# Optimization experiments

Measured on AMD Instinct MI355X. Metric: run time of the kernel, lower is better.

The kernel has to match this reference:

```python
import jax, jax.numpy as jnp
import numpy as np

# (left, right, top, bottom) zero-pad offsets for the 8 neighbors (matches nn.ZeroPad2d order in source)
PADS = [(0, 2, 0, 2), (1, 1, 0, 2), (2, 0, 0, 2), (0, 2, 1, 1),
        (2, 0, 1, 1), (0, 2, 2, 0), (1, 1, 2, 0), (2, 0, 2, 0)]
CROP_H = [96, 128, 160, 192]
CROP_W = [192, 256, 320, 384]
PROP_TIME = 3


def _shift_pad8(x):
    # x: [B,1,h,w] -> [B,8,h+2,w+2], each channel a differently shifted zero-padded copy
    xs = [jnp.pad(x[:, 0], ((0, 0), (t, b), (l, r))) for (l, r, t, b) in PADS]
    return jnp.stack(xs, axis=1)


def _cspn(guidance, blur_depth, sparse_depth):
    # guidance: [B,8,h,w]; blur_depth/sparse_depth: [B,1,h,w]. norm_type='8sum'.
    gates = [jnp.pad(guidance[:, k], ((0, 0), (t, b), (l, r)))
             for k, (l, r, t, b) in enumerate(PADS)]
    gate_wb = jnp.stack(gates, axis=1)                              # [B,8,h+2,w+2]
    abs_weight = jnp.sum(jnp.abs(gate_wb), axis=1, keepdims=True)   # [B,1,h+2,w+2]
    gate_wb = gate_wb / abs_weight
    gate_sum = jnp.sum(gate_wb, axis=1, keepdims=True)[:, :, 1:-1, 1:-1]  # [B,1,h,w]

    sparse_mask = jnp.sign(sparse_depth)
    raw = blur_depth
    result = blur_depth
    for i in range(PROP_TIME):
        if i == 0:
            result = (1.0 - sparse_mask) * result + sparse_mask * sparse_depth
        neigh = jnp.sum(gate_wb * _shift_pad8(result), axis=1, keepdims=True)
        result = (1.0 - gate_sum) * raw + neigh[:, :, 1:-1, 1:-1]
    return result


def _conv_block(x, w, b):
    # ConvBlock (monodepth2 style): reflection pad 1 + 3x3 conv + ELU
    xp = jnp.pad(x, ((0, 0), (0, 0), (1, 1), (1, 1)), mode='reflect')
    y = jax.lax.conv_general_dilated(xp, w, (1, 1), 'VALID',
                                     dimension_numbers=('NCHW', 'OIHW', 'NCHW'))
    return jax.nn.elu(y + b[None, :, None, None])


def _center_crop(x, h, w):
    oh, ow = x.shape[2], x.shape[3]
    hs = max(int(round((oh - h) / 2)), 0)
    ws = max(int(round((ow - w) / 2)), 0)
    return x[:, :, hs:min(hs + h, oh), ws:min(ws + w, ow)]


def _stage_pad(depth, h, w):
    hs, ws = depth.shape[2], depth.shape[3]
    ph, pw = (h - hs) // 2, (w - ws) // 2
    return jnp.pad(depth, ((0, 0), (0, 0), (ph, ph), (pw, pw)))


def _masked_median(x, mask):
    # torch.median semantics: lower median of the masked elements
    s = jnp.sort(jnp.where(mask, x, jnp.inf).ravel())
    n = jnp.sum(mask)
    return jnp.take(s, (n - 1) // 2)


def _stage_forward(features, rgbd, dep_last, w, b, h, wd):
    rgbd_c = _center_crop(rgbd, h, wd)
    feat_c = _center_crop(features, h, wd)
    dep = rgbd_c[:, 0:1]                       # channel 0, as in source
    mask = jnp.sign(dep_last)
    dep_fusion = dep_last * mask + dep * (1.0 - mask)
    guided_map = _conv_block(feat_c, w, b)     # [B,8,h,wd]
    x = _cspn(guided_map, dep_fusion, dep_last)
    return jnp.clip(x, 0.0, 1.0)


def setup_inputs() -> dict:
    key = jax.random.key(0)
    ks = jax.random.split(key, 12)
    B, H, W = 16, 256, 512
    inp = {
        'features': jax.random.normal(ks[0], (B, 16, H, W), jnp.float32),
        'blur_depth': jax.random.uniform(ks[1], (B, 1, H, W), jnp.float32),
        'gt': jax.random.uniform(ks[2], (B, 1, H, W), jnp.float32),
        'rgb': jax.random.uniform(ks[3], (B, 3, H, W), jnp.float32),
        'stage': jnp.arange(4, dtype=jnp.int64 if jax.config.jax_enable_x64 else jnp.int32),
    }
    scale = 1.0 / np.sqrt(16 * 9)
    for i in range(4):
        inp[f'w{i}'] = jax.random.normal(ks[4 + i], (8, 16, 3, 3), jnp.float32) * scale
        inp[f'b{i}'] = jax.random.normal(ks[8 + i], (8,), jnp.float32) * 0.01
    return inp


def reference(features, blur_depth, gt, rgb, w0, b0, w1, b1, w2, b2, w3, b3, stage):
    stage_list = [int(s) for s in np.asarray(stage)]
    gt_pos = gt > 0
    scale = _masked_median(gt, gt_pos) / _masked_median(blur_depth, gt_pos)
    all_scale = gt / blur_depth
    blur_depth_o = blur_depth * scale
    gt = jnp.where((all_scale > 1.2) | (all_scale < 0.8), 0.0, gt)
    rgbd = jnp.concatenate([rgb, blur_depth_o], axis=1)
    dep_last = _center_crop(gt, 96, 192)

    params = [(w0, b0), (w1, b1), (w2, b2), (w3, b3)]
    out = None
    for index, i in enumerate(stage_list):
        w, b = params[i]
        if index == len(stage_list) - 1:
            out = _stage_forward(features, rgbd, dep_last, w, b, CROP_H[i], CROP_W[i])
        else:
            ref_last = jax.lax.stop_gradient(
                _stage_forward(features, rgbd, dep_last, w, b, CROP_H[i], CROP_W[i]))
            dep_last = _stage_pad(ref_last, CROP_H[i + 1], CROP_W[i + 1])
    return out
```

## Files before the change

kernel.cpp:

```cpp
#include <hip/hip_runtime.h>
#include <math.h>


#define B 16
#define FH 256
#define FW 512
#define TH 32
#define TW 32
#define HALO 3
#define LD 38
#define GD 36
#define MAXC 6

typedef __attribute__((ext_vector_type(8))) short short8;
typedef __attribute__((ext_vector_type(4))) float f32x4;

__device__ __forceinline__ int swzslot(int cc, int h) {
  return (((cc << 1) | h) ^ (cc & 1) ^ ((cc >> 1) & 2));
}

__global__ __launch_bounds__(256) void prep_all_kernel(
    const float* __restrict__ gt, const float* __restrict__ blur,
    const float* __restrict__ rgb, const float* __restrict__ w0c,
    const float* __restrict__ w1c, const float* __restrict__ w2c,
    const float* __restrict__ w3c, short8* __restrict__ wf,
    float* __restrict__ r0, float* __restrict__ r1, float* __restrict__ r2,
    float* __restrict__ r3) {
  if (blockIdx.x == 0 && threadIdx.x < 64) {
    int lane = threadIdx.x;
    int px = lane & 15, g = lane >> 4;
    const float* Ws[4] = {w0c, w1c, w2c, w3c};
    for (int st = 0; st < 4; ++st) {
      const float* wgt = Ws[st];
      for (int t = 0; t < 5; ++t) {
        short8 wh, wl;
        for (int j = 0; j < 8; ++j) {
          int k = 32 * t + 8 * g + j;
          int s = k >> 4, ci = k & 15;
          float wv = 0.0f;
          if (px < 8 && s < 9) wv = wgt[(px * 16 + ci) * 9 + s];
          uint uw = __float_as_uint(wv);
          uint hw_ = (uw + 0x8000u) & 0xFFFF0000u;
          float wlo = wv - __uint_as_float(hw_);
          wh[j] = (short)(hw_ >> 16);
          wl[j] = (short)((__float_as_uint(wlo) + 0x8000u) >> 16);
        }
        wf[((st * 5 + t) * 2 + 0) * 64 + lane] = wh;
        wf[((st * 5 + t) * 2 + 1) * 64 + lane] = wl;
      }
    }
  }

  int idx = blockIdx.x * blockDim.x + threadIdx.x;
  const int n0 = B * 96 * 192, n1 = B * 128 * 256, n2 = B * 160 * 320,
            n3 = B * 192 * 384;
  float* dst;
  int h, w, hs, ws;
  if (idx < n0) {
    dst = r0; h = 96; w = 192; hs = 80; ws = 160;
  } else if (idx < n0 + n1) {
    idx -= n0; dst = r1; h = 128; w = 256; hs = 64; ws = 128;
  } else if (idx < n0 + n1 + n2) {
    idx -= n0 + n1; dst = r2; h = 160; w = 320; hs = 48; ws = 96;
  } else if (idx < n0 + n1 + n2 + n3) {
    idx -= n0 + n1 + n2; dst = r3; h = 192; w = 384; hs = 32; ws = 64;
  } else {
    return;
  }
  int x = idx % w;
  int t = idx / w;
  int y = t % h;
  int b = t / h;
  size_t g = (size_t)b * FH * FW + (size_t)(hs + y) * FW + (ws + x);
  float dep = rgb[((size_t)b * 3) * FH * FW + (size_t)(hs + y) * FW + (ws + x)];
  if (dst == r0) {
    float gv = gt[g];
    float s = gv / blur[g];
    float dl = (s > 1.2f || s < 0.8f) ? 0.0f : gv;
    dst[idx] = (dl > 0.0f) ? dl : dep;
  } else {
    dst[idx] = dep;
  }
}

__global__ __launch_bounds__(256) void conv_mfma_kernel(
    const float* __restrict__ feat, const short8* __restrict__ wf,
    const float* __restrict__ b0c, float* __restrict__ g0,
    const float* __restrict__ b1c, float* __restrict__ g1,
    const float* __restrict__ b2c, float* __restrict__ g2,
    const float* __restrict__ b3c, float* __restrict__ g3) {
  __shared__ uint4 sH[18 * 72];
  __shared__ uint4 sL[18 * 72];

  int bid = blockIdx.x;
  int h, w, base, st;
  const float* bias;
  float* guid;
  if (bid < 576)       { h = 96;  w = 192; bias = b0c; guid = g0; base = 0;    st = 0; }
  else if (bid < 1600) { h = 128; w = 256; bias = b1c; guid = g1; base = 576;  st = 1; }
  else if (bid < 3200) { h = 160; w = 320; bias = b2c; guid = g2; base = 1600; st = 2; }
  else                 { h = 192; w = 384; bias = b3c; guid = g3; base = 3200; st = 3; }
  int hs = (FH - h) >> 1, wss = (FW - w) >> 1;

  int lb = bid - base;
  int nbx = w >> 5;
  int bx = lb % nbx;
  int rem = lb / nbx;
  int nby = h >> 4;
  int by = rem % nby;
  int b = rem / nby;
  int tx0 = bx << 5, ty0 = by << 4;

  int tid = threadIdx.x;
  int lane = tid & 63, wv = tid >> 6;
  int px = lane & 15, g = lane >> 4;
  int h_ = g & 1, gb = g >> 1;

  const short8* wfs = wf + st * 640;
  short8 WH[5], WL[5];
#pragma unroll
  for (int t = 0; t < 5; ++t) {
    WH[t] = wfs[(t * 2 + 0) * 64 + lane];
    WL[t] = wfs[(t * 2 + 1) * 64 + lane];
  }
  float bias4[4];
  {
    const float* bp = bias + ((g & 1) << 2);
#pragma unroll
    for (int r = 0; r < 4; ++r) bias4[r] = bp[r];
  }

  const size_t FHW = (size_t)FH * FW;
  const float* fb = feat + (size_t)b * 16 * FHW;
  for (int u = tid; u < 612; u += 256) {
    int rr = u / 34, cc = u % 34;
    int yy = ty0 + rr - 1;
    yy = (yy < 0) ? 1 : ((yy >= h) ? h - 2 : yy);
    int xx = tx0 + cc - 1;
    xx = (xx < 0) ? 1 : ((xx >= w) ? w - 2 : xx);
    const float* fp = fb + (size_t)(hs + yy) * FW + (wss + xx);
    uint hiD[8], loD[8];
#pragma unroll
    for (int i = 0; i < 8; ++i) {
      float a0 = fp[(size_t)(2 * i) * FHW];
      float a1 = fp[(size_t)(2 * i + 1) * FHW];
      uint u0 = __float_as_uint(a0), u1 = __float_as_uint(a1);
      uint h0 = (u0 + 0x8000u) & 0xFFFF0000u;
      uint h1 = (u1 + 0x8000u) & 0xFFFF0000u;
      float l0 = a0 - __uint_as_float(h0);
      float l1 = a1 - __uint_as_float(h1);
      hiD[i] = (h0 >> 16) | h1;
      loD[i] = ((__float_as_uint(l0) + 0x8000u) >> 16) |
               (((__float_as_uint(l1) + 0x8000u) >> 16) << 16);
    }
    int r72 = rr * 72;
    sH[r72 + swzslot(cc, 0)] = make_uint4(hiD[0], hiD[1], hiD[2], hiD[3]);
    sH[r72 + swzslot(cc, 1)] = make_uint4(hiD[4], hiD[5], hiD[6], hiD[7]);
    sL[r72 + swzslot(cc, 0)] = make_uint4(loD[0], loD[1], loD[2], loD[3]);
    sL[r72 + swzslot(cc, 1)] = make_uint4(loD[4], loD[5], loD[6], loD[7]);
  }
  __syncthreads();

  size_t hw = (size_t)h * w;
  const short8* pH = (const short8*)sH;
  const short8* pL = (const short8*)sL;

  const int dyE_[5] = {-1, -1, 0, 1, 1};
  const int dxE_[5] = {-1, 1, 0, -1, 1};
  const int dyO_[5] = {-1, 0, 0, 1, 0};
  const int dxO_[5] = {0, -1, 1, 0, 0};

  for (int i = 0; i < 8; ++i) {
    int tau = wv * 8 + i;
    int row = tau >> 1, xt = tau & 1;
    int rr0 = row + 1;
    int cc0 = (xt << 4) + px + 1;
    f32x4 acc = {bias4[0], bias4[1], bias4[2], bias4[3]};
#pragma unroll
    for (int t = 0; t < 5; ++t) {
      int dy = gb ? dyO_[t] : dyE_[t];
      int dx = gb ? dxO_[t] : dxE_[t];
      int idx = (rr0 + dy) * 72 + swzslot(cc0 + dx, h_);
      short8 fh = pH[idx];
      short8 fl = pL[idx];
      acc = __builtin_amdgcn_mfma_f32_16x16x32_bf16(WH[t], fh, acc, 0, 0, 0);
      acc = __builtin_amdgcn_mfma_f32_16x16x32_bf16(WH[t], fl, acc, 0, 0, 0);
      acc = __builtin_amdgcn_mfma_f32_16x16x32_bf16(WL[t], fh, acc, 0, 0, 0);
    }
    if (g < 2) {
      int y = ty0 + row, x = tx0 + (xt << 4) + px;
      float* gp = guid + (size_t)b * 8 * hw + (size_t)y * w + x;
#pragma unroll
      for (int r = 0; r < 4; ++r) {
        int oo = g * 4 + r;
        float v = acc[r];
        v = (v > 0.0f) ? v : (__expf(v) - 1.0f);
        gp[(size_t)oo * hw] = v;
      }
    }
  }
}

__global__ __launch_bounds__(256) void cspn3_kernel(
    const float* __restrict__ guid, const float* __restrict__ raw,
    const float* __restrict__ rgb, float* __restrict__ dst, int h, int w,
    int hs, int wss, int h2, int w2, int ph, int pw, int last) {
  __shared__ float sraw[LD * LD];
  __shared__ float s0[LD * LD];
  __shared__ float s1[LD * LD];

  int tpw = w / TW, tph = h / TH;
  int tile = blockIdx.x;
  int tx = tile % tpw;
  int t2 = tile / tpw;
  int ty = t2 % tph;
  int b = t2 / tph;
  int oy = ty * TH - HALO, ox = tx * TW - HALO;
  int tid = threadIdx.x;

  const float* rb = raw + (size_t)b * h * w;

  for (int e = tid; e < LD * LD; e += 256) {
    int r = e / LD, c = e % LD;
    int gy = oy + r, gx = ox + c;
    bool in = (gy >= 0 && gy < h && gx >= 0 && gx < w);
    sraw[e] = in ? rb[(size_t)gy * w + gx] : 0.0f;
  }
  __syncthreads();

  const int dy8[8] = {1, 1, 1, 0, 0, -1, -1, -1};
  const int dx8[8] = {1, 0, -1, 1, -1, 1, 0, -1};
  const int off8[8] = {LD + 1, LD, LD - 1, 1, -1, -LD + 1, -LD, -LD - 1};

  const float* gb = guid + (size_t)b * 8 * h * w;
  float cg[MAXC][8];
  float r0[MAXC];
  int adr[MAXC];
#pragma unroll
  for (int ch = 0; ch < MAXC; ++ch) {
    int p = tid + ch * 256;
    bool ok = p < GD * GD;
    int pp = ok ? p : 0;
    int py = pp / GD + 1, px = pp % GD + 1;
    adr[ch] = py * LD + px;
    int gy = oy + py, gx = ox + px;
    bool in = ok && gy >= 0 && gy < h && gx >= 0 && gx < w;
    float wsum = 0.0f, asum = 0.0f;
    float g[8];
#pragma unroll
    for (int k = 0; k < 8; ++k) {
      int ny = gy + dy8[k], nx = gx + dx8[k];
      bool nin = ok && ny >= 0 && ny < h && nx >= 0 && nx < w;
      float gk = nin ? gb[(size_t)k * h * w + (size_t)ny * w + nx] : 0.0f;
      g[k] = gk;
      wsum += gk;
      asum += fabsf(gk);
    }
    float inv = in ? (1.0f / asum) : 0.0f;
#pragma unroll
    for (int k = 0; k < 8; ++k) cg[ch][k] = g[k] * inv;
    r0[ch] = in ? (1.0f - wsum * inv) * sraw[adr[ch]] : 0.0f;
  }

#pragma unroll
  for (int ch = 0; ch < MAXC; ++ch) {
    int p = tid + ch * 256;
    if (p < GD * GD) {
      float v = r0[ch];
#pragma unroll
      for (int k = 0; k < 8; ++k) v += cg[ch][k] * sraw[adr[ch] + off8[k]];
      s0[adr[ch]] = v;
    }
  }
  __syncthreads();

#pragma unroll
  for (int ch = 0; ch < MAXC; ++ch) {
    int p = tid + ch * 256;
    if (p < GD * GD) {
      int py = p / GD + 1, px = p % GD + 1;
      if (py >= 2 && py <= 35 && px >= 2 && px <= 35) {
        float v = r0[ch];
#pragma unroll
        for (int k = 0; k < 8; ++k) v += cg[ch][k] * s0[adr[ch] + off8[k]];
        s1[adr[ch]] = v;
      }
    }
  }
  __syncthreads();

#pragma unroll
  for (int ch = 0; ch < MAXC; ++ch) {
    int p = tid + ch * 256;
    if (p < GD * GD) {
      int py = p / GD + 1, px = p % GD + 1;
      if (py >= 3 && py <= 34 && px >= 3 && px <= 34) {
        float v = r0[ch];
#pragma unroll
        for (int k = 0; k < 8; ++k) v += cg[ch][k] * s1[adr[ch] + off8[k]];
        float dl = fminf(fmaxf(v, 0.0f), 1.0f);
        int gy = oy + py, gx = ox + px;
        if (last) {
          dst[((size_t)b * h + gy) * w + gx] = dl;
        } else {
          float dep = rgb[((size_t)b * 3) * FH * FW + (size_t)(hs + gy) * FW +
                          (wss + gx)];
          dst[((size_t)b * h2 + (gy + ph)) * w2 + (gx + pw)] =
              (dl > 0.0f) ? dl : dep;
        }
      }
    }
  }
}

extern "C" void kernel_launch(void* const* d_in, const int* in_sizes, int n_in,
                              void* d_out, int out_size, void* d_ws,
                              size_t ws_size, hipStream_t stream) {
  (void)in_sizes; (void)n_in; (void)out_size; (void)ws_size;
  const float* feat = (const float*)d_in[0];
  const float* blur = (const float*)d_in[1];
  const float* gt = (const float*)d_in[2];
  const float* rgb = (const float*)d_in[3];
  const float* W[4] = {(const float*)d_in[5], (const float*)d_in[7],
                       (const float*)d_in[9], (const float*)d_in[11]};
  const float* Bs[4] = {(const float*)d_in[6], (const float*)d_in[8],
                        (const float*)d_in[10], (const float*)d_in[12]};
  float* out = (float*)d_out;

  float* G0 = (float*)d_ws;
  float* G1 = G0 + (size_t)B * 8 * 96 * 192;
  float* G2 = G1 + (size_t)B * 8 * 128 * 256;
  float* G3 = G2 + (size_t)B * 8 * 160 * 320;
  float* RAW[4];
  RAW[0] = G3 + (size_t)B * 8 * 192 * 384;
  RAW[1] = RAW[0] + (size_t)B * 96 * 192;
  RAW[2] = RAW[1] + (size_t)B * 128 * 256;
  RAW[3] = RAW[2] + (size_t)B * 160 * 320;
  short8* WF = (short8*)(RAW[3] + (size_t)B * 192 * 384);
  float* G[4] = {G0, G1, G2, G3};

  const int CH[4] = {96, 128, 160, 192};
  const int CW[4] = {192, 256, 320, 384};

  {
    int n = B * (96 * 192 + 128 * 256 + 160 * 320 + 192 * 384);
    prep_all_kernel<<<(n + 255) / 256, 256, 0, stream>>>(
        gt, blur, rgb, W[0], W[1], W[2], W[3], WF, RAW[0], RAW[1], RAW[2],
        RAW[3]);
  }

  conv_mfma_kernel<<<5504, 256, 0, stream>>>(feat, WF, Bs[0], G0, Bs[1], G1,
                                             Bs[2], G2, Bs[3], G3);

  for (int i = 0; i < 4; ++i) {
    int h = CH[i], w = CW[i];
    int hs = (FH - h) / 2, wss = (FW - w) / 2;
    int ntiles = B * (h / TH) * (w / TW);
    if (i < 3) {
      int h2 = CH[i + 1], w2 = CW[i + 1];
      int ph = (h2 - h) / 2, pw = (w2 - w) / 2;
      cspn3_kernel<<<ntiles, 256, 0, stream>>>(G[i], RAW[i], rgb, RAW[i + 1],
                                               h, w, hs, wss, h2, w2, ph, pw,
                                               0);
    } else {
      cspn3_kernel<<<ntiles, 256, 0, stream>>>(G[i], RAW[i], rgb, out, h, w,
                                               hs, wss, h, w, 0, 0, 1);
    }
  }
}
```

Before: 183.9 us.

## Share feature tile loads across all four stage convolutions

The conv kernel now launches one block per tile of the largest 192x384 crop instead of separate blocks per stage. Each block loads and splits the feature halo into shared memory once, then runs the convolution for every stage whose crop fully contains the tile. Reflection padding at each stage's borders is handled by remapping neighbour indices inside the stencil. This removes redundant global feature reads across the nested crops, but central blocks now do up to four convolutions each, so work per block becomes uneven.

Result: faster. 173.2 us (-5.8%).

```diff
diff --git a/kernel.cpp b/kernel.cpp
--- a/kernel.cpp
+++ b/kernel.cpp
@@ -93,52 +93,26 @@
   __shared__ uint4 sL[18 * 72];
 
   int bid = blockIdx.x;
-  int h, w, base, st;
-  const float* bias;
-  float* guid;
-  if (bid < 576)       { h = 96;  w = 192; bias = b0c; guid = g0; base = 0;    st = 0; }
-  else if (bid < 1600) { h = 128; w = 256; bias = b1c; guid = g1; base = 576;  st = 1; }
-  else if (bid < 3200) { h = 160; w = 320; bias = b2c; guid = g2; base = 1600; st = 2; }
-  else                 { h = 192; w = 384; bias = b3c; guid = g3; base = 3200; st = 3; }
-  int hs = (FH - h) >> 1, wss = (FW - w) >> 1;
-
-  int lb = bid - base;
-  int nbx = w >> 5;
-  int bx = lb % nbx;
-  int rem = lb / nbx;
-  int nby = h >> 4;
-  int by = rem % nby;
-  int b = rem / nby;
-  int tx0 = bx << 5, ty0 = by << 4;
+  int bx = bid % 12;
+  int t0 = bid / 12;
+  int by = t0 % 12;
+  int b = t0 / 12;
+  int ty0 = by << 4, tx0 = bx << 5;
 
   int tid = threadIdx.x;
   int lane = tid & 63, wv = tid >> 6;
   int px = lane & 15, g = lane >> 4;
   int h_ = g & 1, gb = g >> 1;
-
-  const short8* wfs = wf + st * 640;
-  short8 WH[5], WL[5];
-#pragma unroll
-  for (int t = 0; t < 5; ++t) {
-    WH[t] = wfs[(t * 2 + 0) * 64 + lane];
-    WL[t] = wfs[(t * 2 + 1) * 64 + lane];
-  }
-  float bias4[4];
-  {
-    const float* bp = bias + ((g & 1) << 2);
-#pragma unroll
-    for (int r = 0; r < 4; ++r) bias4[r] = bp[r];
-  }
 
   const size_t FHW = (size_t)FH * FW;
   const float* fb = feat + (size_t)b * 16 * FHW;
   for (int u = tid; u < 612; u += 256) {
     int rr = u / 34, cc = u % 34;
     int yy = ty0 + rr - 1;
-    yy = (yy < 0) ? 1 : ((yy >= h) ? h - 2 : yy);
+    yy = (yy < 0) ? 0 : ((yy > 191) ? 191 : yy);
     int xx = tx0 + cc - 1;
-    xx = (xx < 0) ? 1 : ((xx >= w) ? w - 2 : xx);
-    const float* fp = fb + (size_t)(hs + yy) * FW + (wss + xx);
+    xx = (xx < 0) ? 0 : ((xx > 383) ? 383 : xx);
+    const float* fp = fb + (size_t)(32 + yy) * FW + (64 + xx);
     uint hiD[8], loD[8];
 #pragma unroll
     for (int i = 0; i < 8; ++i) {
@@ -161,41 +135,78 @@
   }
   __syncthreads();
 
-  size_t hw = (size_t)h * w;
   const short8* pH = (const short8*)sH;
   const short8* pL = (const short8*)sL;
-
   const int dyE_[5] = {-1, -1, 0, 1, 1};
   const int dxE_[5] = {-1, 1, 0, -1, 1};
   const int dyO_[5] = {-1, 0, 0, 1, 0};
   const int dxO_[5] = {0, -1, 1, 0, 0};
 
-  for (int i = 0; i < 8; ++i) {
-    int tau = wv * 8 + i;
-    int row = tau >> 1, xt = tau & 1;
-    int rr0 = row + 1;
-    int cc0 = (xt << 4) + px + 1;
-    f32x4 acc = {bias4[0], bias4[1], bias4[2], bias4[3]};
+  const int SH[4] = {96, 128, 160, 192};
+  const int SW[4] = {192, 256, 320, 384};
+  const int OY[4] = {48, 32, 16, 0};
+  const int OX[4] = {96, 64, 32, 0};
+  const float* BIAS[4] = {b0c, b1c, b2c, b3c};
+  float* GD_[4] = {g0, g1, g2, g3};
+
+#pragma unroll
+  for (int st = 0; st < 4; ++st) {
+    int sh = SH[st], sw = SW[st], oy = OY[st], ox = OX[st];
+    bool inR = (ty0 >= oy) && (ty0 + 16 <= oy + sh) && (tx0 >= ox) &&
+               (tx0 + 32 <= ox + sw);
+    if (!inR) continue;
+    bool topE = (ty0 == oy), botE = (ty0 + 16 == oy + sh);
+    bool leftE = (tx0 == ox), rightE = (tx0 + 32 == ox + sw);
+
+    const short8* wfs = wf + st * 640;
+    short8 WH[5], WL[5];
 #pragma unroll
     for (int t = 0; t < 5; ++t) {
-      int dy = gb ? dyO_[t] : dyE_[t];
-      int dx = gb ? dxO_[t] : dxE_[t];
-      int idx = (rr0 + dy) * 72 + swzslot(cc0 + dx, h_);
-      short8 fh = pH[idx];
-      short8 fl = pL[idx];
-      acc = __builtin_amdgcn_mfma_f32_16x16x32_bf16(WH[t], fh, acc, 0, 0, 0);
-      acc = __builtin_amdgcn_mfma_f32_16x16x32_bf16(WH[t], fl, acc, 0, 0, 0);
-      acc = __builtin_amdgcn_mfma_f32_16x16x32_bf16(WL[t], fh, acc, 0, 0, 0);
-    }
-    if (g < 2) {
-      int y = ty0 + row, x = tx0 + (xt << 4) + px;
-      float* gp = guid + (size_t)b * 8 * hw + (size_t)y * w + x;
-#pragma unroll
-      for (int r = 0; r < 4; ++r) {
-        int oo = g * 4 + r;
-        float v = acc[r];
-        v = (v > 0.0f) ? v : (__expf(v) - 1.0f);
-        gp[(size_t)oo * hw] = v;
+      WH[t] = wfs[(t * 2 + 0) * 64 + lane];
+      WL[t] = wfs[(t * 2 + 1) * 64 + lane];
+    }
+    float bias4[4];
+    {
+      const float* bp = BIAS[st] + ((g & 1) << 2);
+#pragma unroll
+      for (int r = 0; r < 4; ++r) bias4[r] = bp[r];
+    }
+    size_t hw = (size_t)sh * sw;
+    float* guid = GD_[st];
+
+    for (int i = 0; i < 8; ++i) {
+      int tau = wv * 8 + i;
+      int row = tau >> 1, xt = tau & 1;
+      int rr0 = row + 1;
+      int cc0 = (xt << 4) + px + 1;
+      f32x4 acc = {bias4[0], bias4[1], bias4[2], bias4[3]};
+#pragma unroll
+      for (int t = 0; t < 5; ++t) {
+        int dy = gb ? dyO_[t] : dyE_[t];
+        int dx = gb ? dxO_[t] : dxE_[t];
+        int rr = rr0 + dy;
+        if (dy < 0 && topE && row == 0) rr = rr0 + 1;
+        if (dy > 0 && botE && row == 15) rr = rr0 - 1;
+        int cc = cc0 + dx;
+        if (dx < 0 && leftE && cc0 == 1) cc = cc0 + 1;
+        if (dx > 0 && rightE && cc0 == 32) cc = cc0 - 1;
+        int idx = rr * 72 + swzslot(cc, h_);
+        short8 fh = pH[idx];
+        short8 fl = pL[idx];
+        acc = __builtin_amdgcn_mfma_f32_16x16x32_bf16(WH[t], fh, acc, 0, 0, 0);
+        acc = __builtin_amdgcn_mfma_f32_16x16x32_bf16(WH[t], fl, acc, 0, 0, 0);
+        acc = __builtin_amdgcn_mfma_f32_16x16x32_bf16(WL[t], fh, acc, 0, 0, 0);
+      }
+      if (g < 2) {
+        int ly = ty0 + row - oy, lx = tx0 + (xt << 4) + px - ox;
+        float* gp = guid + (size_t)b * 8 * hw + (size_t)ly * sw + lx;
+#pragma unroll
+        for (int r = 0; r < 4; ++r) {
+          int oo = g * 4 + r;
+          float v = acc[r];
+          v = (v > 0.0f) ? v : (__expf(v) - 1.0f);
+          gp[(size_t)oo * hw] = v;
+        }
       }
     }
   }
@@ -349,7 +360,7 @@
         RAW[3]);
   }
 
-  conv_mfma_kernel<<<5504, 256, 0, stream>>>(feat, WF, Bs[0], G0, Bs[1], G1,
+  conv_mfma_kernel<<<2304, 256, 0, stream>>>(feat, WF, Bs[0], G0, Bs[1], G1,
                                              Bs[2], G2, Bs[3], G3);
 
   for (int i = 0; i < 4; ++i) {
```
